# Optimization experiments

Measured on AMD Instinct MI355X. Metric: run time of the kernel, lower is better.

Reference implementation:

```python
import jax, jax.numpy as jnp
import numpy as np

N_EMBD = 768
N_HEADS = 12
HEAD_DIM = N_EMBD // N_HEADS
B, T = 2, 4096


def setup_inputs() -> dict:
    key = jax.random.key(0)
    k1, k2, k3 = jax.random.split(key, 3)
    x = jax.random.normal(k1, (B, T, N_EMBD), dtype=jnp.float32)
    # torch Linear(in, out) weight has shape (out, in); x @ W.T == x @ W_j with W_j = W.T
    w_qkv = jax.random.normal(k2, (N_EMBD, 3 * N_EMBD), dtype=jnp.float32) * (1.0 / np.sqrt(N_EMBD))
    w_proj = jax.random.normal(k3, (N_EMBD, N_EMBD), dtype=jnp.float32) * (1.0 / np.sqrt(N_EMBD))
    return {"x": x, "w_qkv": w_qkv, "w_proj": w_proj}


def reference(x, w_qkv, w_proj):
    Bx, Tx, C = x.shape
    qkv = x @ w_qkv                                  # [B,T,3C]
    q, k, v = jnp.split(qkv, 3, axis=2)
    def to_heads(t):
        return t.reshape(Bx, Tx, N_HEADS, HEAD_DIM).transpose(0, 2, 1, 3)  # [B,H,T,D]
    q, k, v = to_heads(q), to_heads(k), to_heads(v)
    scale = HEAD_DIM ** -0.5
    att = jnp.einsum('bhqd,bhkd->bhqk', q, k) * scale  # [B,H,T,T]
    causal = jnp.tril(jnp.ones((Tx, Tx), dtype=bool))
    att = jnp.where(causal[None, None], att, -jnp.inf)
    att = jax.nn.softmax(att, axis=-1)
    y = jnp.einsum('bhqk,bhkd->bhqd', att, v)          # [B,H,T,D]
    y = y.transpose(0, 2, 1, 3).reshape(Bx, Tx, C)
    return y @ w_proj
```

## Files before the change

### kernel.cpp

```cpp
#include <hip/hip_runtime.h>
#include <hip/hip_bf16.h>

#define Bn 2
#define Tn 4096
#define Cn 768
#define Hn 12
#define Dn 64
#define Mn (Bn * Tn)
#define PAD 72

typedef __attribute__((ext_vector_type(8))) short bf16x8;
typedef __attribute__((ext_vector_type(4))) short bf16x4;
typedef __attribute__((ext_vector_type(4))) float f32x4;

typedef const __attribute__((address_space(1))) unsigned int* gas_ptr;
typedef __attribute__((address_space(3))) unsigned int* las_ptr;

__device__ __forceinline__ float b2f(unsigned short u) {
    return __uint_as_float(((unsigned int)u) << 16);
}
__device__ __forceinline__ unsigned short f2b(float f) {
    unsigned int x = __float_as_uint(f);
    x += 0x7FFFu + ((x >> 16) & 1u);
    return (unsigned short)(x >> 16);
}
__device__ __forceinline__ unsigned int cvt_pk_bf16(float lo, float hi) {
    unsigned int r;
    asm("v_cvt_pk_bf16_f32 %0, %1, %2" : "=v"(r) : "v"(lo), "v"(hi));
    return r;
}

__device__ __forceinline__ void async_ld16(const unsigned short* g, unsigned short* l) {
    __builtin_amdgcn_global_load_lds((gas_ptr)(const void*)g, (las_ptr)(void*)l, 16, 0, 0);
}

__global__ void detect_k(const unsigned short* __restrict__ W, int* __restrict__ flag) {
    __shared__ int any;
    if (threadIdx.x == 0) any = 0;
    __syncthreads();
    int4 v = reinterpret_cast<const int4*>(W)[threadIdx.x];
    const unsigned short* u = reinterpret_cast<const unsigned short*>(&v);
    int bad = 0;
#pragma unroll
    for (int j = 0; j < 8; ++j) {
        const unsigned int e = (u[j] >> 7) & 0xFFu;
        bad |= (e >= 0x88u) ? 1 : 0;
    }
    if (bad) atomicOr(&any, 1);
    __syncthreads();
    if (threadIdx.x == 0) *flag = any;
}

__global__ __launch_bounds__(256) void convert_x_k(
    const void* __restrict__ in, unsigned short* __restrict__ out,
    const int* __restrict__ flag)
{
    const size_t i = ((size_t)blockIdx.x * 256 + threadIdx.x) * 8;
    union { int4 v; unsigned short u[8]; } pk;
    if (*flag) {
        const float* p = (const float*)in + i;
        float4 a = *reinterpret_cast<const float4*>(p);
        float4 b = *reinterpret_cast<const float4*>(p + 4);
        float t[8] = {a.x, a.y, a.z, a.w, b.x, b.y, b.z, b.w};
#pragma unroll
        for (int j = 0; j < 8; ++j) pk.u[j] = f2b(t[j]);
    } else {
        pk.v = *reinterpret_cast<const int4*>((const unsigned short*)in + i);
    }
    *reinterpret_cast<int4*>(out + i) = pk.v;
}

__global__ __launch_bounds__(256) void transpose_w_k(
    const void* __restrict__ in, unsigned short* __restrict__ out,
    int K, int N, const int* __restrict__ flag)
{
    __shared__ unsigned short Ts[64][PAD];
    const int tid = threadIdx.x;
    const int kB = blockIdx.y * 64, nB = blockIdx.x * 64;
    const bool f32 = (*flag != 0);
#pragma unroll
    for (int it = 0; it < 2; ++it) {
        const int r = (tid >> 3) + it * 32;
        const int c = (tid & 7) * 8;
        float t[8];
        if (f32) {
            const float* p = (const float*)in + (size_t)(kB + r) * N + nB + c;
            float4 a = *reinterpret_cast<const float4*>(p);
            float4 b = *reinterpret_cast<const float4*>(p + 4);
            t[0]=a.x;t[1]=a.y;t[2]=a.z;t[3]=a.w;t[4]=b.x;t[5]=b.y;t[6]=b.z;t[7]=b.w;
        } else {
            int4 v = *reinterpret_cast<const int4*>((const unsigned short*)in + (size_t)(kB + r) * N + nB + c);
            const unsigned short* u = reinterpret_cast<const unsigned short*>(&v);
#pragma unroll
            for (int j = 0; j < 8; ++j) t[j] = b2f(u[j]);
        }
#pragma unroll
        for (int j = 0; j < 8; ++j) Ts[c + j][r] = f2b(t[j]);
    }
    __syncthreads();
#pragma unroll
    for (int it = 0; it < 2; ++it) {
        const int n = (tid >> 3) + it * 32;
        const int k = (tid & 7) * 8;
        *reinterpret_cast<int4*>(out + (size_t)(nB + n) * K + kB + k) =
            *reinterpret_cast<const int4*>(&Ts[n][k]);
    }
}

__global__ __launch_bounds__(256) void transpose_v_k(
    const unsigned short* __restrict__ Vin, unsigned short* __restrict__ Vt)
{
    __shared__ unsigned short Ts[64][PAD];
    const int tid = threadIdx.x;
    const size_t base = (size_t)blockIdx.y * Tn * Dn;
    const int t0 = blockIdx.x * 64;
#pragma unroll
    for (int it = 0; it < 2; ++it) {
        const int r = (tid >> 3) + it * 32;
        const int c = (tid & 7) * 8;
        int4 vv = *reinterpret_cast<const int4*>(Vin + base + (size_t)(t0 + r) * Dn + c);
        const unsigned short* u = reinterpret_cast<const unsigned short*>(&vv);
#pragma unroll
        for (int j = 0; j < 8; ++j) Ts[c + j][r] = u[j];
    }
    __syncthreads();
#pragma unroll
    for (int it = 0; it < 2; ++it) {
        const int d = (tid >> 3) + it * 32;
        const int tc = (tid & 7) * 8;
        *reinterpret_cast<int4*>(Vt + base + (size_t)d * Tn + t0 + tc) =
            *reinterpret_cast<const int4*>(&Ts[d][tc]);
    }
}

template <int EPI>
__global__ __launch_bounds__(256) void gemm_lds(
    const unsigned short* __restrict__ A, const unsigned short* __restrict__ Bt,
    void* __restrict__ Out, unsigned short* __restrict__ Qo,
    unsigned short* __restrict__ Ko, unsigned short* __restrict__ Vo,
    int M, int N, int K, const int* __restrict__ flag)
{
    __shared__ unsigned short As[8192];
    __shared__ unsigned short Bs[8192];
    const int tid = threadIdx.x;
    const int w = tid >> 6, l = tid & 63;
    const int l15 = l & 15, l4 = l >> 4;
    const int rowBase = blockIdx.y * 128;
    const int colBase = blockIdx.x * 128;
    const int mq = (w & 1) * 64, nq = (w >> 1) * 64;
    const bool f32 = (*flag != 0);

    const int laneRow = l15, laneK = l4 * 8;

    f32x4 acc[4][4];
#pragma unroll
    for (int i = 0; i < 4; ++i)
#pragma unroll
        for (int j = 0; j < 4; ++j) acc[i][j] = (f32x4){0.f, 0.f, 0.f, 0.f};

    for (int k0 = 0; k0 < K; k0 += 64) {
        __syncthreads();
#pragma unroll
        for (int j = 0; j < 4; ++j) {
            const int c = w * 4 + j;
            const int mt_g = c >> 1, kh = c & 1;
            const size_t ga = (size_t)(rowBase + mt_g * 16 + laneRow) * K + k0 + kh * 32 + laneK;
            const size_t gb = (size_t)(colBase + mt_g * 16 + laneRow) * K + k0 + kh * 32 + laneK;
            async_ld16(A + ga, &As[c * 512]);
            async_ld16(Bt + gb, &Bs[c * 512]);
        }
        __syncthreads();

#pragma unroll
        for (int kh = 0; kh < 2; ++kh) {
            bf16x8 af[4], bf[4];
#pragma unroll
            for (int mt = 0; mt < 4; ++mt)
                af[mt] = *reinterpret_cast<const bf16x8*>(
                    &As[(((mq >> 4) + mt) * 2 + kh) * 512 + l * 8]);
#pragma unroll
            for (int nt = 0; nt < 4; ++nt)
                bf[nt] = *reinterpret_cast<const bf16x8*>(
                    &Bs[(((nq >> 4) + nt) * 2 + kh) * 512 + l * 8]);
#pragma unroll
            for (int mt = 0; mt < 4; ++mt)
#pragma unroll
                for (int nt = 0; nt < 4; ++nt)
                    acc[mt][nt] = __builtin_amdgcn_mfma_f32_16x16x32_bf16(af[mt], bf[nt], acc[mt][nt], 0, 0, 0);
        }
    }

#pragma unroll
    for (int mt = 0; mt < 4; ++mt)
#pragma unroll
        for (int i = 0; i < 4; ++i) {
            const int m = rowBase + mq + mt * 16 + l4 * 4 + i;
#pragma unroll
            for (int nt = 0; nt < 4; ++nt) {
                const int n0 = colBase + nq + nt * 16 + l15;
                if (EPI == 0) {
                    if (f32) ((float*)Out)[(size_t)m * N + n0] = acc[mt][nt][i];
                    else ((unsigned short*)Out)[(size_t)m * N + n0] = f2b(acc[mt][nt][i]);
                } else {
                    const int sec = n0 / 768;
                    const int cc = n0 - sec * 768;
                    const int h = cc >> 6, d = cc & 63;
                    const int b = m >> 12, t = m & 4095;
                    unsigned short* dst = (sec == 0) ? Qo : (sec == 1) ? Ko : Vo;
                    dst[(((size_t)(b * Hn + h) * Tn + t) * Dn) + d] = f2b(acc[mt][nt][i]);
                }
            }
        }
}

__global__ __launch_bounds__(256) void gemm_qkv_fb(
    const void* __restrict__ A, const unsigned short* __restrict__ Bt,
    unsigned short* __restrict__ Qo, unsigned short* __restrict__ Ko,
    unsigned short* __restrict__ Vo, int M, int N, int K,
    const int* __restrict__ flag)
{
    __shared__ unsigned short As[128 * PAD];
    __shared__ unsigned short Bs[128 * PAD];
    const int tid = threadIdx.x;
    const int w = tid >> 6, l = tid & 63;
    const int l15 = l & 15, l4 = l >> 4;
    const int rowBase = blockIdx.y * 128;
    const int colBase = blockIdx.x * 128;
    const int mq = (w & 1) * 64, nq = (w >> 1) * 64;
    const bool af32 = (*flag != 0);

    f32x4 acc[4][4];
#pragma unroll
    for (int i = 0; i < 4; ++i)
#pragma unroll
        for (int j = 0; j < 4; ++j) acc[i][j] = (f32x4){0.f, 0.f, 0.f, 0.f};

    for (int k0 = 0; k0 < K; k0 += 64) {
        __syncthreads();
#pragma unroll
        for (int it = 0; it < 4; ++it) {
            const int s = tid + it * 256;
            const int r = s >> 3, c = (s & 7) * 8;
            union { int4 v; unsigned short u[8]; } pk;
            if (af32) {
                const float* p = (const float*)A + (size_t)(rowBase + r) * K + k0 + c;
                float4 a = *reinterpret_cast<const float4*>(p);
                float4 b = *reinterpret_cast<const float4*>(p + 4);
                float t[8] = {a.x, a.y, a.z, a.w, b.x, b.y, b.z, b.w};
#pragma unroll
                for (int j = 0; j < 8; ++j) pk.u[j] = f2b(t[j]);
            } else {
                pk.v = *reinterpret_cast<const int4*>(
                    (const unsigned short*)A + (size_t)(rowBase + r) * K + k0 + c);
            }
            *reinterpret_cast<int4*>(&As[r * PAD + c]) = pk.v;
            *reinterpret_cast<int4*>(&Bs[r * PAD + c]) =
                *reinterpret_cast<const int4*>(Bt + (size_t)(colBase + r) * K + k0 + c);
        }
        __syncthreads();
#pragma unroll
        for (int kk = 0; kk < 64; kk += 32) {
            bf16x8 af[4], bf[4];
#pragma unroll
            for (int mt = 0; mt < 4; ++mt)
                af[mt] = *reinterpret_cast<const bf16x8*>(&As[(mq + mt * 16 + l15) * PAD + kk + l4 * 8]);
#pragma unroll
            for (int nt = 0; nt < 4; ++nt)
                bf[nt] = *reinterpret_cast<const bf16x8*>(&Bs[(nq + nt * 16 + l15) * PAD + kk + l4 * 8]);
#pragma unroll
            for (int mt = 0; mt < 4; ++mt)
#pragma unroll
                for (int nt = 0; nt < 4; ++nt)
                    acc[mt][nt] = __builtin_amdgcn_mfma_f32_16x16x32_bf16(af[mt], bf[nt], acc[mt][nt], 0, 0, 0);
        }
    }

#pragma unroll
    for (int mt = 0; mt < 4; ++mt)
#pragma unroll
        for (int i = 0; i < 4; ++i) {
            const int m = rowBase + mq + mt * 16 + l4 * 4 + i;
#pragma unroll
            for (int nt = 0; nt < 4; ++nt) {
                const int n0 = colBase + nq + nt * 16 + l15;
                const int sec = n0 / 768;
                const int cc = n0 - sec * 768;
                const int h = cc >> 6, d = cc & 63;
                const int b = m >> 12, t = m & 4095;
                unsigned short* dst = (sec == 0) ? Qo : (sec == 1) ? Ko : Vo;
                dst[(((size_t)(b * Hn + h) * Tn + t) * Dn) + d] = f2b(acc[mt][nt][i]);
            }
        }
}

__global__ __launch_bounds__(256, 4) void attn_mfma2(
    const unsigned short* __restrict__ Q, const unsigned short* __restrict__ K,
    const unsigned short* __restrict__ Vt, unsigned short* __restrict__ Y)
{
    __shared__ unsigned short Ks[2][8 * 512];
    __shared__ unsigned short Vs[2][8 * 512];

    const int tid = threadIdx.x;
    const int w = tid >> 6, l = tid & 63;
    const int l15 = l & 15, l4 = l >> 4;

    const int f = (int)blockIdx.y * 32 + (int)blockIdx.x;
    const int r8 = f & 7, j = f >> 3;
    const int bh = r8 * 3 + (j >> 5);
    const int xq = j & 31;

    const size_t base = (size_t)bh * Tn * Dn;
    const float sc = 0.125f * 1.44269504088896f;
    const int b = bh / Hn, h = bh - b * Hn;

    const int vlb = (l4 >> 1) * 256 + l15 * 16 + (l4 & 1) * 8;

    for (int half = 0; half < 2; ++half) {
        const int t = half ? xq : (63 - xq);
        const int q0 = t * 64;
        const int qrow = q0 + w * 16 + l15;

        bf16x8 aq[2];
#pragma unroll
        for (int kh = 0; kh < 2; ++kh)
            aq[kh] = *reinterpret_cast<const bf16x8*>(
                Q + base + (size_t)qrow * Dn + kh * 32 + l4 * 8);

        f32x4 o[4];
#pragma unroll
        for (int dt = 0; dt < 4; ++dt) o[dt] = (f32x4){0.f, 0.f, 0.f, 0.f};
        float lsum = 0.f;

        const int nst = (q0 >> 6) + 1;

        __syncthreads();
#pragma unroll
        for (int jj = 0; jj < 2; ++jj) {
            const int c = w * 2 + jj;
            const int sub = c >> 1, kh = c & 1;
            async_ld16(K + base + (size_t)(sub * 16 + l15) * Dn + kh * 32 + l4 * 8,
                       &Ks[0][c * 512]);
            async_ld16(Vt + base + (size_t)(sub * 16 + l15) * Tn + kh * 32 + l4 * 8,
                       &Vs[0][c * 512]);
        }

        int cur = 0;
        for (int s = 0; s < nst; ++s) {
            const int k0 = s << 6;
            __syncthreads();

            if (s + 1 < nst) {
                const int kn = k0 + 64;
#pragma unroll
                for (int jj = 0; jj < 2; ++jj) {
                    const int c = w * 2 + jj;
                    const int sub = c >> 1, kh = c & 1;
                    async_ld16(K + base + (size_t)(kn + sub * 16 + l15) * Dn + kh * 32 + l4 * 8,
                               &Ks[cur ^ 1][c * 512]);
                    async_ld16(Vt + base + (size_t)(sub * 16 + l15) * Tn + kn + kh * 32 + l4 * 8,
                               &Vs[cur ^ 1][c * 512]);
                }
            }

            f32x4 sfr[4];
#pragma unroll
            for (int tt = 0; tt < 4; ++tt) {
                bf16x8 ak0 = *reinterpret_cast<const bf16x8*>(&Ks[cur][(tt * 2 + 0) * 512 + l * 8]);
                bf16x8 ak1 = *reinterpret_cast<const bf16x8*>(&Ks[cur][(tt * 2 + 1) * 512 + l * 8]);
                f32x4 z = (f32x4){0.f, 0.f, 0.f, 0.f};
                z = __builtin_amdgcn_mfma_f32_16x16x32_bf16(ak0, aq[0], z, 0, 0, 0);
                z = __builtin_amdgcn_mfma_f32_16x16x32_bf16(ak1, aq[1], z, 0, 0, 0);
                sfr[tt] = z;
            }

            const bool need_mask = (k0 + 63 > q0);
            float p[4][4];
#pragma unroll
            for (int tt = 0; tt < 4; ++tt)
#pragma unroll
                for (int i = 0; i < 4; ++i) {
                    float s2 = sfr[tt][i] * sc;
                    if (need_mask && (k0 + tt * 16 + l4 * 4 + i > qrow)) s2 = -1e30f;
                    const float e = exp2f(s2);
                    p[tt][i] = e;
                    lsum += e;
                }

            bf16x4 pa[4];
#pragma unroll
            for (int tt = 0; tt < 4; ++tt) {
                union { unsigned int u[2]; bf16x4 v; } uu;
                uu.u[0] = cvt_pk_bf16(p[tt][0], p[tt][1]);
                uu.u[1] = cvt_pk_bf16(p[tt][2], p[tt][3]);
                pa[tt] = uu.v;
            }

            const char* vb = (const char*)&Vs[cur][0];
#pragma unroll
            for (int dt = 0; dt < 4; ++dt) {
#pragma unroll
                for (int tt = 0; tt < 4; ++tt) {
                    bf16x4 bv = *reinterpret_cast<const bf16x4*>(vb + dt * 2048 + tt * 512 + vlb);
                    o[dt] = __builtin_amdgcn_mfma_f32_16x16x16bf16_1k(pa[tt], bv, o[dt], 0, 0, 0);
                }
            }
            cur ^= 1;
        }

        lsum += __shfl_xor(lsum, 16);
        lsum += __shfl_xor(lsum, 32);

#pragma unroll
        for (int i = 0; i < 4; ++i) {
            const float lv = __shfl(lsum, (l & 48) + (l4 * 4 + i));
            const float inv = 1.0f / lv;
            const int row = q0 + w * 16 + l4 * 4 + i;
#pragma unroll
            for (int dt = 0; dt < 4; ++dt)
                Y[((size_t)(b * Tn + row)) * Cn + h * 64 + dt * 16 + l15] = f2b(o[dt][i] * inv);
        }
    }
}

__global__ __launch_bounds__(256, 3) void attn_mfma_fb(
    const unsigned short* __restrict__ Q, const unsigned short* __restrict__ K,
    const unsigned short* __restrict__ V, unsigned short* __restrict__ Y)
{
    __shared__ unsigned short Ks[96 * PAD];
    __shared__ unsigned short Vtl[96 * PAD];
    __shared__ unsigned short Ps[96 * PAD];

    const int tid = threadIdx.x;
    const int w = tid >> 6, l = tid & 63;
    const int l15 = l & 15, l4 = l >> 4;
    const int bh = blockIdx.y;
    const size_t base = (size_t)bh * Tn * Dn;
    const float sc = 0.125f * 1.44269504088896f;
    const int b = bh / Hn, h = bh - b * Hn;

    for (int half = 0; half < 2; ++half) {
        const int t = half ? (int)blockIdx.x : (63 - (int)blockIdx.x);
        const int q0 = t * 64;

        bf16x8 aq[2];
#pragma unroll
        for (int kh = 0; kh < 2; ++kh)
            aq[kh] = *reinterpret_cast<const bf16x8*>(
                Q + base + (size_t)(q0 + w * 16 + l15) * Dn + kh * 32 + l4 * 8);

        f32x4 o[4];
#pragma unroll
        for (int dt = 0; dt < 4; ++dt) o[dt] = (f32x4){0.f, 0.f, 0.f, 0.f};
        float l_i[4] = {0.f, 0.f, 0.f, 0.f};

        const int kend = q0 + 64;
        for (int k0 = 0; k0 < kend; k0 += 64) {
            __syncthreads();
#pragma unroll
            for (int it = 0; it < 2; ++it) {
                const int s = tid + it * 256;
                const int r = s >> 3, c = (s & 7) * 8;
                *reinterpret_cast<int4*>(&Ks[r * PAD + c]) =
                    *reinterpret_cast<const int4*>(K + base + (size_t)(k0 + r) * Dn + c);
            }
#pragma unroll
            for (int it = 0; it < 2; ++it) {
                const int r = tid & 63, d0 = (tid >> 6) * 8 + it * 32;
                int4 vv = *reinterpret_cast<const int4*>(V + base + (size_t)(k0 + r) * Dn + d0);
                const unsigned short* vu = reinterpret_cast<const unsigned short*>(&vv);
#pragma unroll
                for (int j = 0; j < 8; ++j) Vtl[(d0 + j) * PAD + r] = vu[j];
            }
            __syncthreads();

            f32x4 sfr[4];
#pragma unroll
            for (int tt = 0; tt < 4; ++tt) {
                bf16x8 bk0 = *reinterpret_cast<const bf16x8*>(&Ks[(tt * 16 + l15) * PAD + l4 * 8]);
                bf16x8 bk1 = *reinterpret_cast<const bf16x8*>(&Ks[(tt * 16 + l15) * PAD + 32 + l4 * 8]);
                f32x4 z = (f32x4){0.f, 0.f, 0.f, 0.f};
                z = __builtin_amdgcn_mfma_f32_16x16x32_bf16(aq[0], bk0, z, 0, 0, 0);
                z = __builtin_amdgcn_mfma_f32_16x16x32_bf16(aq[1], bk1, z, 0, 0, 0);
                sfr[tt] = z;
            }

            const bool need_mask = (k0 + 63 > q0);
            float p[4][4];
#pragma unroll
            for (int tt = 0; tt < 4; ++tt) {
                const int cb = k0 + tt * 16 + l15;
                const int rb = q0 + w * 16 + l4 * 4;
#pragma unroll
                for (int i = 0; i < 4; ++i) {
                    float s = sfr[tt][i] * sc;
                    if (need_mask && (cb > rb + i)) s = -1e30f;
                    const float e = exp2f(s);
                    p[tt][i] = e;
                    l_i[i] += e;
                }
            }

#pragma unroll
            for (int tt = 0; tt < 4; ++tt)
#pragma unroll
                for (int i = 0; i < 4; ++i)
                    Ps[(w * 16 + l4 * 4 + i) * PAD + tt * 16 + l15] = f2b(p[tt][i]);

            bf16x8 ap0 = *reinterpret_cast<const bf16x8*>(&Ps[(w * 16 + l15) * PAD + l4 * 8]);
            bf16x8 ap1 = *reinterpret_cast<const bf16x8*>(&Ps[(w * 16 + l15) * PAD + 32 + l4 * 8]);
#pragma unroll
            for (int dt = 0; dt < 4; ++dt) {
                bf16x8 bv0 = *reinterpret_cast<const bf16x8*>(&Vtl[(dt * 16 + l15) * PAD + l4 * 8]);
                bf16x8 bv1 = *reinterpret_cast<const bf16x8*>(&Vtl[(dt * 16 + l15) * PAD + 32 + l4 * 8]);
                o[dt] = __builtin_amdgcn_mfma_f32_16x16x32_bf16(ap0, bv0, o[dt], 0, 0, 0);
                o[dt] = __builtin_amdgcn_mfma_f32_16x16x32_bf16(ap1, bv1, o[dt], 0, 0, 0);
            }
        }

#pragma unroll
        for (int i = 0; i < 4; ++i)
#pragma unroll
            for (int off = 1; off < 16; off <<= 1) l_i[i] += __shfl_xor(l_i[i], off);

#pragma unroll
        for (int i = 0; i < 4; ++i) {
            const float inv = 1.0f / l_i[i];
            const int row = q0 + w * 16 + l4 * 4 + i;
#pragma unroll
            for (int dt = 0; dt < 4; ++dt)
                Y[((size_t)(b * Tn + row)) * Cn + h * 64 + dt * 16 + l15] = f2b(o[dt][i] * inv);
        }
    }
}

extern "C" void kernel_launch(void* const* d_in, const int* in_sizes, int n_in,
                              void* d_out, int out_size, void* d_ws, size_t ws_size,
                              hipStream_t stream)
{
    const void* x = d_in[0];
    const void* wqkv = d_in[1];
    const void* wproj = d_in[2];
    const size_t HSZ = (size_t)Bn * Hn * Tn * Dn;
    unsigned short* q = (unsigned short*)d_ws;
    unsigned short* k = q + HSZ;
    unsigned short* v = k + HSZ;
    unsigned short* R = v + HSZ;
    unsigned short* wqkvT = R;
    unsigned short* y = R;
    unsigned short* wprojT = q;
    const bool big = ws_size >= (size_t)5 * HSZ * 2 + 16;
    unsigned short* xb = R + HSZ;
    unsigned short* vt = xb;
    int* flag = big ? (int*)(xb + HSZ) : (int*)(R + HSZ);

    detect_k<<<1, 256, 0, stream>>>((const unsigned short*)wqkv, flag);
    transpose_w_k<<<dim3(3 * Cn / 64, Cn / 64), 256, 0, stream>>>(wqkv, wqkvT, Cn, 3 * Cn, flag);
    if (big) {
        convert_x_k<<<(Mn * Cn) / (256 * 8), 256, 0, stream>>>(x, xb, flag);
        gemm_lds<1><<<dim3(3 * Cn / 128, Mn / 128), 256, 0, stream>>>(
            xb, wqkvT, nullptr, q, k, v, Mn, 3 * Cn, Cn, flag);
        transpose_v_k<<<dim3(Tn / 64, Bn * Hn), 256, 0, stream>>>(v, vt);
        attn_mfma2<<<dim3(Tn / 128, Bn * Hn), 256, 0, stream>>>(q, k, vt, y);
    } else {
        gemm_qkv_fb<<<dim3(3 * Cn / 128, Mn / 128), 256, 0, stream>>>(
            x, wqkvT, q, k, v, Mn, 3 * Cn, Cn, flag);
        attn_mfma_fb<<<dim3(Tn / 128, Bn * Hn), 256, 0, stream>>>(q, k, v, y);
    }
    transpose_w_k<<<dim3(Cn / 64, Cn / 64), 256, 0, stream>>>(wproj, wprojT, Cn, Cn, flag);
    gemm_lds<0><<<dim3(Cn / 128, Mn / 128), 256, 0, stream>>>(
        y, wprojT, d_out, nullptr, nullptr, nullptr, Mn, Cn, Cn, flag);
}
```

Baseline: 327.3 us.

## Split attention key range across two wave groups with 512-thread blocks

The attention kernel now runs 8 waves per block. Two groups of four waves each handle half of a 128-key step for the same 64 query rows, and their partial outputs and row sums are merged through shared memory at the end. The goal is more waves in flight and better latency hiding on the causal key loop. In exchange, V is now single-buffered and loaded synchronously each step, which adds an extra barrier per step, and the final reduction adds another LDS pass.

New measurement: 338.0 us. 1.03x slower.

```diff
diff --git a/kernel.cpp b/kernel.cpp
--- a/kernel.cpp
+++ b/kernel.cpp
@@ -293,15 +293,16 @@
         }
 }
 
-__global__ __launch_bounds__(256, 4) void attn_mfma2(
+__global__ __launch_bounds__(512, 6) void attn_mfma3(
     const unsigned short* __restrict__ Q, const unsigned short* __restrict__ K,
     const unsigned short* __restrict__ Vt, unsigned short* __restrict__ Y)
 {
-    __shared__ unsigned short Ks[2][8 * 512];
-    __shared__ unsigned short Vs[2][8 * 512];
+    __shared__ unsigned short Ks[2][16 * 512];
+    __shared__ unsigned short Vs[16 * 512];
 
     const int tid = threadIdx.x;
     const int w = tid >> 6, l = tid & 63;
+    const int g = w >> 2, wq = w & 3;
     const int l15 = l & 15, l4 = l >> 4;
 
     const int f = (int)blockIdx.y * 32 + (int)blockIdx.x;
@@ -315,10 +316,12 @@
 
     const int vlb = (l4 >> 1) * 256 + l15 * 16 + (l4 & 1) * 8;
 
+    float* scr = reinterpret_cast<float*>(&Ks[0][0]);
+
     for (int half = 0; half < 2; ++half) {
         const int t = half ? xq : (63 - xq);
         const int q0 = t * 64;
-        const int qrow = q0 + w * 16 + l15;
+        const int qrow = q0 + wq * 16 + l15;
 
         bf16x8 aq[2];
 #pragma unroll
@@ -331,7 +334,7 @@
         for (int dt = 0; dt < 4; ++dt) o[dt] = (f32x4){0.f, 0.f, 0.f, 0.f};
         float lsum = 0.f;
 
-        const int nst = (q0 >> 6) + 1;
+        const int nst = (t + 2) >> 1;
 
         __syncthreads();
 #pragma unroll
@@ -340,84 +343,114 @@
             const int sub = c >> 1, kh = c & 1;
             async_ld16(K + base + (size_t)(sub * 16 + l15) * Dn + kh * 32 + l4 * 8,
                        &Ks[0][c * 512]);
-            async_ld16(Vt + base + (size_t)(sub * 16 + l15) * Tn + kh * 32 + l4 * 8,
-                       &Vs[0][c * 512]);
         }
 
         int cur = 0;
         for (int s = 0; s < nst; ++s) {
-            const int k0 = s << 6;
+            const int k0 = s << 7;
             __syncthreads();
 
             if (s + 1 < nst) {
-                const int kn = k0 + 64;
+                const int kn = k0 + 128;
 #pragma unroll
                 for (int jj = 0; jj < 2; ++jj) {
                     const int c = w * 2 + jj;
                     const int sub = c >> 1, kh = c & 1;
                     async_ld16(K + base + (size_t)(kn + sub * 16 + l15) * Dn + kh * 32 + l4 * 8,
                                &Ks[cur ^ 1][c * 512]);
-                    async_ld16(Vt + base + (size_t)(sub * 16 + l15) * Tn + kn + kh * 32 + l4 * 8,
-                               &Vs[cur ^ 1][c * 512]);
                 }
             }
-
-            f32x4 sfr[4];
-#pragma unroll
-            for (int tt = 0; tt < 4; ++tt) {
-                bf16x8 ak0 = *reinterpret_cast<const bf16x8*>(&Ks[cur][(tt * 2 + 0) * 512 + l * 8]);
-                bf16x8 ak1 = *reinterpret_cast<const bf16x8*>(&Ks[cur][(tt * 2 + 1) * 512 + l * 8]);
-                f32x4 z = (f32x4){0.f, 0.f, 0.f, 0.f};
-                z = __builtin_amdgcn_mfma_f32_16x16x32_bf16(ak0, aq[0], z, 0, 0, 0);
-                z = __builtin_amdgcn_mfma_f32_16x16x32_bf16(ak1, aq[1], z, 0, 0, 0);
-                sfr[tt] = z;
-            }
-
-            const bool need_mask = (k0 + 63 > q0);
-            float p[4][4];
-#pragma unroll
-            for (int tt = 0; tt < 4; ++tt)
-#pragma unroll
-                for (int i = 0; i < 4; ++i) {
-                    float s2 = sfr[tt][i] * sc;
-                    if (need_mask && (k0 + tt * 16 + l4 * 4 + i > qrow)) s2 = -1e30f;
-                    const float e = exp2f(s2);
-                    p[tt][i] = e;
-                    lsum += e;
+            {
+#pragma unroll
+                for (int jj = 0; jj < 2; ++jj) {
+                    const int c = w * 2 + jj;
+                    const int dt = c >> 2, kq = c & 3;
+                    async_ld16(Vt + base + (size_t)(dt * 16 + l15) * Tn + k0 + kq * 32 + l4 * 8,
+                               &Vs[c * 512]);
                 }
-
+            }
+
+            const int gk0 = k0 + g * 64;
+            const bool live = (gk0 <= q0 + 63);
             bf16x4 pa[4];
-#pragma unroll
-            for (int tt = 0; tt < 4; ++tt) {
-                union { unsigned int u[2]; bf16x4 v; } uu;
-                uu.u[0] = cvt_pk_bf16(p[tt][0], p[tt][1]);
-                uu.u[1] = cvt_pk_bf16(p[tt][2], p[tt][3]);
-                pa[tt] = uu.v;
-            }
-
-            const char* vb = (const char*)&Vs[cur][0];
-#pragma unroll
-            for (int dt = 0; dt < 4; ++dt) {
+            if (live) {
+                f32x4 sfr[4];
 #pragma unroll
                 for (int tt = 0; tt < 4; ++tt) {
-                    bf16x4 bv = *reinterpret_cast<const bf16x4*>(vb + dt * 2048 + tt * 512 + vlb);
-                    o[dt] = __builtin_amdgcn_mfma_f32_16x16x16bf16_1k(pa[tt], bv, o[dt], 0, 0, 0);
+                    bf16x8 ak0 = *reinterpret_cast<const bf16x8*>(
+                        &Ks[cur][((g * 4 + tt) * 2 + 0) * 512 + l * 8]);
+                    bf16x8 ak1 = *reinterpret_cast<const bf16x8*>(
+                        &Ks[cur][((g * 4 + tt) * 2 + 1) * 512 + l * 8]);
+                    f32x4 z = (f32x4){0.f, 0.f, 0.f, 0.f};
+                    z = __builtin_amdgcn_mfma_f32_16x16x32_bf16(ak0, aq[0], z, 0, 0, 0);
+                    z = __builtin_amdgcn_mfma_f32_16x16x32_bf16(ak1, aq[1], z, 0, 0, 0);
+                    sfr[tt] = z;
                 }
+
+                const bool need_mask = (gk0 + 63 > q0);
+#pragma unroll
+                for (int tt = 0; tt < 4; ++tt) {
+                    float e[4];
+#pragma unroll
+                    for (int i = 0; i < 4; ++i) {
+                        float s2 = sfr[tt][i] * sc;
+                        if (need_mask && (gk0 + tt * 16 + l4 * 4 + i > qrow)) s2 = -1e30f;
+                        e[i] = exp2f(s2);
+                        lsum += e[i];
+                    }
+                    union { unsigned int u[2]; bf16x4 v; } uu;
+                    uu.u[0] = cvt_pk_bf16(e[0], e[1]);
+                    uu.u[1] = cvt_pk_bf16(e[2], e[3]);
+                    pa[tt] = uu.v;
+                }
+            }
+
+            __syncthreads();
+
+            if (live) {
+                const char* vb = (const char*)&Vs[0] + g * 2048;
+#pragma unroll
+                for (int tt = 0; tt < 4; ++tt) {
+#pragma unroll
+                    for (int dt = 0; dt < 4; ++dt) {
+                        bf16x4 bv = *reinterpret_cast<const bf16x4*>(vb + dt * 4096 + tt * 512 + vlb);
+                        o[dt] = __builtin_amdgcn_mfma_f32_16x16x16bf16_1k(pa[tt], bv, o[dt], 0, 0, 0);
+                    }
+                }
             }
             cur ^= 1;
         }
 
-        lsum += __shfl_xor(lsum, 16);
-        lsum += __shfl_xor(lsum, 32);
-
-#pragma unroll
-        for (int i = 0; i < 4; ++i) {
-            const float lv = __shfl(lsum, (l & 48) + (l4 * 4 + i));
-            const float inv = 1.0f / lv;
-            const int row = q0 + w * 16 + l4 * 4 + i;
+        __syncthreads();
+        if (g == 1) {
 #pragma unroll
             for (int dt = 0; dt < 4; ++dt)
-                Y[((size_t)(b * Tn + row)) * Cn + h * 64 + dt * 16 + l15] = f2b(o[dt][i] * inv);
+#pragma unroll
+                for (int i = 0; i < 4; ++i)
+                    scr[wq * 1024 + l * 16 + dt * 4 + i] = o[dt][i];
+            scr[4096 + wq * 64 + l] = lsum;
+        }
+        __syncthreads();
+        if (g == 0) {
+#pragma unroll
+            for (int dt = 0; dt < 4; ++dt)
+#pragma unroll
+                for (int i = 0; i < 4; ++i)
+                    o[dt][i] += scr[wq * 1024 + l * 16 + dt * 4 + i];
+            lsum += scr[4096 + wq * 64 + l];
+
+            lsum += __shfl_xor(lsum, 16);
+            lsum += __shfl_xor(lsum, 32);
+
+#pragma unroll
+            for (int i = 0; i < 4; ++i) {
+                const float lv = __shfl(lsum, (l & 48) + (l4 * 4 + i));
+                const float inv = 1.0f / lv;
+                const int row = q0 + wq * 16 + l4 * 4 + i;
+#pragma unroll
+                for (int dt = 0; dt < 4; ++dt)
+                    Y[((size_t)(b * Tn + row)) * Cn + h * 64 + dt * 16 + l15] = f2b(o[dt][i] * inv);
+            }
         }
     }
 }
@@ -560,7 +593,7 @@
         gemm_lds<1><<<dim3(3 * Cn / 128, Mn / 128), 256, 0, stream>>>(
             xb, wqkvT, nullptr, q, k, v, Mn, 3 * Cn, Cn, flag);
         transpose_v_k<<<dim3(Tn / 64, Bn * Hn), 256, 0, stream>>>(v, vt);
-        attn_mfma2<<<dim3(Tn / 128, Bn * Hn), 256, 0, stream>>>(q, k, vt, y);
+        attn_mfma3<<<dim3(Tn / 128, Bn * Hn), 512, 0, stream>>>(q, k, vt, y);
     } else {
         gemm_qkv_fb<<<dim3(3 * Cn / 128, Mn / 128), 256, 0, stream>>>(
             x, wqkvT, q, k, v, Mn, 3 * Cn, Cn, flag);
```
